# Kernel tuning notes

Hardware: AMD Instinct MI355X
Metric: run time of the kernel (lower is better)

## Reference

```python
import jax, jax.numpy as jnp
import numpy as np

DT = 1.0
TAU_MEM_INV = 0.05
V_LEAK = 0.0
V_TH = 1.0
ALPHA = 100.0  # norse SuperSpike surrogate slope


@jax.custom_vjp
def spike_fn(x):
    # heaviside forward, SuperSpike surrogate backward (norse default 'super')
    return (x > 0).astype(x.dtype)

def _spike_fwd(x):
    return spike_fn(x), x

def _spike_bwd(x, g):
    return (g / (ALPHA * jnp.abs(x) + 1.0) ** 2,)

spike_fn.defvjp(_spike_fwd, _spike_bwd)


def setup_inputs() -> dict:
    key = jax.random.key(0)
    ks = jax.random.split(key, 7)
    T, B = 100, 256
    sizes = [784, 64, 64, 10]
    inp = jax.random.normal(ks[0], (T, B, 1, sizes[0]), dtype=jnp.float32)
    out = {"inp": inp}
    for i in range(3):
        fan_in = sizes[i]
        out[f"W{i}"] = jax.random.normal(ks[1 + 2 * i], (sizes[i + 1], fan_in), dtype=jnp.float32) * (1.0 / np.sqrt(fan_in)).astype(np.float32)
        out[f"b{i}"] = jax.random.normal(ks[2 + 2 * i], (sizes[i + 1],), dtype=jnp.float32) * 0.01
    return out


def _snn_forward(inp, Ws, bs):
    x_seq = inp.squeeze(2)  # [T, B, 784]
    B = x_seq.shape[1]
    v0 = tuple(jnp.zeros((B, W.shape[0]), x_seq.dtype) for W in Ws)

    def step(vs, x):
        new_vs = []
        layer_sp = []
        for W, b, v in zip(Ws, bs, vs):
            i_cur = x @ W.T + b                                  # [B, out]
            v = v + DT * TAU_MEM_INV * (V_LEAK - v + i_cur)      # leaky integrate
            z = spike_fn(v - V_TH)                               # fire
            v = v - z * V_TH                                     # reset_subtract
            x = z
            new_vs.append(v)
            layer_sp.append(z.reshape(-1))                       # x.flatten() per layer
        return tuple(new_vs), (x, jnp.concatenate(layer_sp))

    _, (out_spikes, layer_spikes) = jax.lax.scan(step, v0, x_seq)
    # out_spikes: [T, B, 10]; layer_spikes flattened time-major like torch.cat(list)
    return out_spikes, layer_spikes.reshape(-1)


def reference(inp, W0, b0, W1, b1, W2, b2):
    return _snn_forward(inp, (W0, W1, W2), (b0, b1, b2))
```

## Files before the change

kernel.cpp:

```cpp
#include <hip/hip_runtime.h>

#define T_STEPS 100
#define BATCH 256
#define NIN 784
#define N0 64
#define N1 64
#define N2 10
#define CHUNK (BATCH*N0 + BATCH*N1 + BATCH*N2)
#define KPAD 800
#define WPLANE (N0*KPAD)
#define I0ELEMS (25600*64)

typedef __attribute__((ext_vector_type(8))) short short8;
typedef __attribute__((ext_vector_type(4))) float f32x4;

__device__ inline short bf16_rne(float x) {
  unsigned u = __float_as_uint(x);
  unsigned h = (u + 0x7FFFu + ((u >> 16) & 1u)) >> 16;
  return (short)h;
}
__device__ inline float bf16_val(short h) {
  return __uint_as_float(((unsigned)(unsigned short)h) << 16);
}

__global__ __launch_bounds__(256) void prep_w0(
    const float* __restrict__ W0, short* __restrict__ W0s) {
  int idx = blockIdx.x * 256 + threadIdx.x;
  int col = idx / KPAD, k = idx - col * KPAD;
  float w = (k < NIN) ? W0[col * NIN + k] : 0.0f;
  short h0 = bf16_rne(w);
  float r1 = w - bf16_val(h0);
  short h1 = bf16_rne(r1);
  float r2 = r1 - bf16_val(h1);
  short h2 = bf16_rne(r2);
  W0s[idx]              = h0;
  W0s[WPLANE + idx]     = h1;
  W0s[2 * WPLANE + idx] = h2;
}

__global__ __launch_bounds__(256, 3) void gemm0_kernel(
    const float* __restrict__ X, const short* __restrict__ W0s,
    const float* __restrict__ b0, float* __restrict__ I0T) {
  __shared__ float red[4][32][68];

  const int tid = threadIdx.x;
  const int r0  = blockIdx.x * 32;
  const int wid = tid >> 6;
  const int l   = tid & 63;
  const int lr  = l & 15;
  const int lk  = l >> 4;

  const int kbeg = wid * 192;
  const int ccnt = (wid < 3) ? 6 : 7;

  f32x4 acc[2][4];
#pragma unroll
  for (int rt = 0; rt < 2; ++rt)
#pragma unroll
    for (int ct = 0; ct < 4; ++ct) acc[rt][ct] = f32x4{0.f, 0.f, 0.f, 0.f};

  const float*  xr0 = X + (size_t)(r0 + lr) * NIN;
  const float*  xr1 = xr0 + 16 * NIN;
  const short8* wp  = (const short8*)W0s;

  for (int c = 0; c < ccnt; ++c) {
    const int kb = kbeg + c * 32;
    const int k0 = kb + lk * 8;

    float4 xa0, xb0, xa1, xb1;
    if (k0 < NIN) {
      xa0 = *(const float4*)(xr0 + k0);
      xb0 = *(const float4*)(xr0 + k0 + 4);
      xa1 = *(const float4*)(xr1 + k0);
      xb1 = *(const float4*)(xr1 + k0 + 4);
    } else {
      xa0 = xb0 = xa1 = xb1 = float4{0.f, 0.f, 0.f, 0.f};
    }

    short8 a0[3], a1[3];
    {
      float xs0[8] = {xa0.x, xa0.y, xa0.z, xa0.w, xb0.x, xb0.y, xb0.z, xb0.w};
      float xs1[8] = {xa1.x, xa1.y, xa1.z, xa1.w, xb1.x, xb1.y, xb1.z, xb1.w};
#pragma unroll
      for (int e = 0; e < 8; ++e) {
        float x  = xs0[e];
        short h0 = bf16_rne(x);   float rr1 = x - bf16_val(h0);
        short h1 = bf16_rne(rr1); float rr2 = rr1 - bf16_val(h1);
        a0[0][e] = h0; a0[1][e] = h1; a0[2][e] = bf16_rne(rr2);
        x  = xs1[e];
        h0 = bf16_rne(x);   rr1 = x - bf16_val(h0);
        h1 = bf16_rne(rr1); rr2 = rr1 - bf16_val(h1);
        a1[0][e] = h0; a1[1][e] = h1; a1[2][e] = bf16_rne(rr2);
      }
    }

    const int kof = kb / 8 + lk;
#pragma unroll
    for (int ct = 0; ct < 4; ++ct) {
      const size_t col = (size_t)(ct * 16 + lr);
      short8 bf0 = wp[        col * 100 + kof];
      short8 bf1 = wp[ 6400 + col * 100 + kof];
      short8 bf2 = wp[12800 + col * 100 + kof];
      {
        f32x4 a = acc[0][ct];
        a = __builtin_amdgcn_mfma_f32_16x16x32_bf16(a0[2], bf0, a, 0, 0, 0);
        a = __builtin_amdgcn_mfma_f32_16x16x32_bf16(a0[0], bf2, a, 0, 0, 0);
        a = __builtin_amdgcn_mfma_f32_16x16x32_bf16(a0[1], bf1, a, 0, 0, 0);
        a = __builtin_amdgcn_mfma_f32_16x16x32_bf16(a0[1], bf0, a, 0, 0, 0);
        a = __builtin_amdgcn_mfma_f32_16x16x32_bf16(a0[0], bf1, a, 0, 0, 0);
        a = __builtin_amdgcn_mfma_f32_16x16x32_bf16(a0[0], bf0, a, 0, 0, 0);
        acc[0][ct] = a;
      }
      {
        f32x4 a = acc[1][ct];
        a = __builtin_amdgcn_mfma_f32_16x16x32_bf16(a1[2], bf0, a, 0, 0, 0);
        a = __builtin_amdgcn_mfma_f32_16x16x32_bf16(a1[0], bf2, a, 0, 0, 0);
        a = __builtin_amdgcn_mfma_f32_16x16x32_bf16(a1[1], bf1, a, 0, 0, 0);
        a = __builtin_amdgcn_mfma_f32_16x16x32_bf16(a1[1], bf0, a, 0, 0, 0);
        a = __builtin_amdgcn_mfma_f32_16x16x32_bf16(a1[0], bf1, a, 0, 0, 0);
        a = __builtin_amdgcn_mfma_f32_16x16x32_bf16(a1[0], bf0, a, 0, 0, 0);
        acc[1][ct] = a;
      }
    }
  }

#pragma unroll
  for (int rt = 0; rt < 2; ++rt)
#pragma unroll
    for (int ct = 0; ct < 4; ++ct)
#pragma unroll
      for (int r = 0; r < 4; ++r)
        red[wid][rt * 16 + lk * 4 + r][ct * 16 + lr] = acc[rt][ct][r];
  __syncthreads();

  const int t0  = r0 >> 8;
  const int bb0 = r0 & 255;
  for (int idx = tid; idx < 32 * 16; idx += 256) {
    int row = idx >> 4, q = idx & 15;
    float4 v  = *(const float4*)&red[0][row][q * 4];
    float4 u1 = *(const float4*)&red[1][row][q * 4];
    float4 u2 = *(const float4*)&red[2][row][q * 4];
    float4 u3 = *(const float4*)&red[3][row][q * 4];
    v.x += u1.x; v.y += u1.y; v.z += u1.z; v.w += u1.w;
    v.x += u2.x; v.y += u2.y; v.z += u2.z; v.w += u2.w;
    v.x += u3.x; v.y += u3.y; v.z += u3.z; v.w += u3.w;
    float4 bv = ((const float4*)b0)[q];
    v.x += bv.x; v.y += bv.y; v.z += bv.z; v.w += bv.w;
    ((float4*)I0T)[((size_t)(bb0 + row) * T_STEPS + t0) * 16 + q] = v;
  }
}

__global__ __launch_bounds__(256) void fused_kernel(
    const float* __restrict__ I0T,
    const float* __restrict__ W1, const float* __restrict__ b1,
    const float* __restrict__ W2, const float* __restrict__ b2,
    float* __restrict__ out) {
  __shared__ float bufA[112][68];
  __shared__ float sW1t[64][68];
  __shared__ float sW2[N2][68];
  __shared__ float sI2[T_STEPS][N2];

  const int b   = blockIdx.x;
  const int tid = threadIdx.x;
  const int j   = tid & 63;
  const int tq  = tid >> 6;
  float* outSpk = out;
  float* laySpk = out + T_STEPS * BATCH * N2;

  {
    const float4* src = (const float4*)I0T + (size_t)b * (T_STEPS * 16);
    for (int idx = tid; idx < T_STEPS * 16; idx += 256) {
      float4 v = src[idx];
      int t = idx >> 4, j4 = idx & 15;
      *(float4*)&bufA[t][j4 * 4] = v;
    }
  }
  __syncthreads();

  if (tq == 0) {
    float v = 0.0f;
#pragma unroll
    for (int g = 0; g < 4; ++g) {
      float ic[25];
#pragma unroll
      for (int i = 0; i < 25; ++i) ic[i] = bufA[g * 25 + i][j];
#pragma unroll
      for (int i = 0; i < 25; ++i) {
        v = v + 0.05f * ((0.0f - v) + ic[i]);
        float z = (v > 1.0f) ? 1.0f : 0.0f;
        v -= z;
        ic[i] = z;
      }
#pragma unroll
      for (int i = 0; i < 25; ++i) bufA[g * 25 + i][j] = ic[i];
    }
  } else {
    for (int idx = tid - 64; idx < 64 * 16; idx += 192) {
      int i = idx >> 4, jv = idx & 15;
      float4 wv = *(const float4*)(W1 + (size_t)i * 64 + jv * 4);
      sW1t[jv * 4 + 0][i] = wv.x;
      sW1t[jv * 4 + 1][i] = wv.y;
      sW1t[jv * 4 + 2][i] = wv.z;
      sW1t[jv * 4 + 3][i] = wv.w;
    }
    for (int idx = tid - 64; idx < N2 * 16; idx += 192) {
      int o = idx >> 4, jv = idx & 15;
      *(float4*)&sW2[o][jv * 4] = *(const float4*)(W2 + (size_t)o * 64 + jv * 4);
    }
  }
  __syncthreads();

  for (int idx = tid; idx < T_STEPS * 16; idx += 256) {
    int t = idx >> 4, jv = idx & 15;
    *(float4*)(laySpk + (size_t)t * CHUNK + b * 64 + jv * 4) =
        *(const float4*)&bufA[t][jv * 4];
  }

  const int iq = tid & 15;
  const int ts = tid >> 4;
  float g1[4][7];
  {
    float4 bias = *(const float4*)(b1 + iq * 4);
#pragma unroll
    for (int tt = 0; tt < 7; ++tt) {
      g1[0][tt] = bias.x; g1[1][tt] = bias.y; g1[2][tt] = bias.z; g1[3][tt] = bias.w;
    }
#pragma unroll
    for (int jq = 0; jq < 16; ++jq) {
      float4 z4[7];
#pragma unroll
      for (int tt = 0; tt < 7; ++tt)
        z4[tt] = *(const float4*)&bufA[ts * 7 + tt][jq * 4];
      float4 w4[4];
#pragma unroll
      for (int e = 0; e < 4; ++e)
        w4[e] = *(const float4*)&sW1t[jq * 4 + e][iq * 4];
#pragma unroll
      for (int e = 0; e < 4; ++e) {
#pragma unroll
        for (int tt = 0; tt < 7; ++tt) {
          float zv = ((const float*)&z4[tt])[e];
          g1[0][tt] = fmaf(zv, w4[e].x, g1[0][tt]);
          g1[1][tt] = fmaf(zv, w4[e].y, g1[1][tt]);
          g1[2][tt] = fmaf(zv, w4[e].z, g1[2][tt]);
          g1[3][tt] = fmaf(zv, w4[e].w, g1[3][tt]);
        }
      }
    }
  }
  __syncthreads();
#pragma unroll
  for (int tt = 0; tt < 7; ++tt) {
    float4 o = {g1[0][tt], g1[1][tt], g1[2][tt], g1[3][tt]};
    *(float4*)&bufA[ts * 7 + tt][iq * 4] = o;
  }
  __syncthreads();

  if (tq == 0) {
    float v = 0.0f;
#pragma unroll
    for (int g = 0; g < 4; ++g) {
      float ic[25];
#pragma unroll
      for (int i = 0; i < 25; ++i) ic[i] = bufA[g * 25 + i][j];
#pragma unroll
      for (int i = 0; i < 25; ++i) {
        v = v + 0.05f * ((0.0f - v) + ic[i]);
        float z = (v > 1.0f) ? 1.0f : 0.0f;
        v -= z;
        ic[i] = z;
      }
#pragma unroll
      for (int i = 0; i < 25; ++i) bufA[g * 25 + i][j] = ic[i];
    }
  }
  __syncthreads();

  for (int idx = tid; idx < T_STEPS * 16; idx += 256) {
    int t = idx >> 4, jv = idx & 15;
    *(float4*)(laySpk + (size_t)t * CHUNK + BATCH * N0 + b * 64 + jv * 4) =
        *(const float4*)&bufA[t][jv * 4];
  }

  for (int idx = tid; idx < T_STEPS * N2; idx += 256) {
    int t = idx / N2, o = idx % N2;
    float a = b2[o];
#pragma unroll
    for (int jq = 0; jq < 16; ++jq) {
      float4 z = *(const float4*)&bufA[t][jq * 4];
      float4 wv = *(const float4*)&sW2[o][jq * 4];
      a += z.x * wv.x;
      a += z.y * wv.y;
      a += z.z * wv.z;
      a += z.w * wv.w;
    }
    sI2[t][o] = a;
  }
  __syncthreads();

  if (tid < N2) {
    float v = 0.0f;
#pragma unroll
    for (int g = 0; g < 4; ++g) {
      float ic[25];
#pragma unroll
      for (int i = 0; i < 25; ++i) ic[i] = sI2[g * 25 + i][tid];
#pragma unroll
      for (int i = 0; i < 25; ++i) {
        v = v + 0.05f * ((0.0f - v) + ic[i]);
        float z = (v > 1.0f) ? 1.0f : 0.0f;
        v -= z;
        ic[i] = z;
      }
#pragma unroll
      for (int i = 0; i < 25; ++i) sI2[g * 25 + i][tid] = ic[i];
    }
  }
  __syncthreads();

  for (int idx = tid; idx < T_STEPS * N2; idx += 256) {
    int t = idx / N2, o = idx % N2;
    float z = sI2[t][o];
    outSpk[(size_t)t * (BATCH * N2) + b * N2 + o] = z;
    laySpk[(size_t)t * CHUNK + BATCH * (N0 + N1) + b * N2 + o] = z;
  }
}

extern "C" void kernel_launch(void* const* d_in, const int* in_sizes, int n_in,
                              void* d_out, int out_size, void* d_ws, size_t ws_size,
                              hipStream_t stream) {
  const float* inp = (const float*)d_in[0];
  const float* W0  = (const float*)d_in[1];
  const float* b0  = (const float*)d_in[2];
  const float* W1  = (const float*)d_in[3];
  const float* b1  = (const float*)d_in[4];
  const float* W2  = (const float*)d_in[5];
  const float* b2  = (const float*)d_in[6];

  float* I0T = (float*)d_ws;
  short* W0s = (short*)(I0T + I0ELEMS);

  prep_w0<<<dim3(200), dim3(256), 0, stream>>>(W0, W0s);
  gemm0_kernel<<<dim3(800), dim3(256), 0, stream>>>(inp, W0s, b0, I0T);
  fused_kernel<<<dim3(BATCH), dim3(256), 0, stream>>>(I0T, W1, b1, W2, b2,
                                                      (float*)d_out);
}
```

Baseline: 62.31 us.

## Pre-pack W0 into MFMA fragment order and stage split X tiles through LDS

W0 is pre-split into three bf16 planes laid out in the exact per-lane MFMA fragment order, so each B-fragment load is one contiguous coalesced short8 per lane. The X rows are loaded with coalesced float4 accesses, split into bf16 hi/mid/lo parts, and written to a per-wave LDS tile. The next chunk's global load is issued before the MFMAs as a register prefetch. This adds LDS traffic and drops the occupancy hint on the launch bounds.

```diff
diff --git a/kernel.cpp b/kernel.cpp
--- a/kernel.cpp
+++ b/kernel.cpp
@@ -8,10 +8,14 @@
 #define N2 10
 #define CHUNK (BATCH*N0 + BATCH*N1 + BATCH*N2)
 #define KPAD 800
-#define WPLANE (N0*KPAD)
+#define NCH 25
 #define I0ELEMS (25600*64)
+#define AROW 40
+#define ASPL (32*AROW)
+#define AWAVE (3*ASPL)
 
 typedef __attribute__((ext_vector_type(8))) short short8;
+typedef __attribute__((ext_vector_type(4))) short short4v;
 typedef __attribute__((ext_vector_type(4))) float f32x4;
 
 __device__ inline short bf16_rne(float x) {
@@ -23,26 +27,32 @@
   return __uint_as_float(((unsigned)(unsigned short)h) << 16);
 }
 
-__global__ __launch_bounds__(256) void prep_w0(
-    const float* __restrict__ W0, short* __restrict__ W0s) {
+__global__ __launch_bounds__(256) void prep_w0_pack(
+    const float* __restrict__ W0, short* __restrict__ W0p) {
   int idx = blockIdx.x * 256 + threadIdx.x;
-  int col = idx / KPAD, k = idx - col * KPAD;
+  int e  = idx & 7;
+  int r1 = idx >> 3;
+  int l  = r1 & 63;
+  int r2 = r1 >> 6;
+  int ct = r2 & 3;
+  int r3 = r2 >> 2;
+  int p  = r3 % 3;
+  int c  = r3 / 3;
+  int k   = c * 32 + (l >> 4) * 8 + e;
+  int col = ct * 16 + (l & 15);
   float w = (k < NIN) ? W0[col * NIN + k] : 0.0f;
   short h0 = bf16_rne(w);
-  float r1 = w - bf16_val(h0);
-  short h1 = bf16_rne(r1);
-  float r2 = r1 - bf16_val(h1);
-  short h2 = bf16_rne(r2);
-  W0s[idx]              = h0;
-  W0s[WPLANE + idx]     = h1;
-  W0s[2 * WPLANE + idx] = h2;
-}
-
-__global__ __launch_bounds__(256, 3) void gemm0_kernel(
-    const float* __restrict__ X, const short* __restrict__ W0s,
+  float rr1 = w - bf16_val(h0);
+  short h1 = bf16_rne(rr1);
+  float rr2 = rr1 - bf16_val(h1);
+  short h2 = bf16_rne(rr2);
+  W0p[idx] = (p == 0) ? h0 : (p == 1) ? h1 : h2;
+}
+
+__global__ __launch_bounds__(256) void gemm0_kernel(
+    const float* __restrict__ X, const short* __restrict__ W0p,
     const float* __restrict__ b0, float* __restrict__ I0T) {
-  __shared__ float red[4][32][68];
-
+  __shared__ __align__(16) char smem[4 * 32 * 68 * 4];
   const int tid = threadIdx.x;
   const int r0  = blockIdx.x * 32;
   const int wid = tid >> 6;
@@ -50,8 +60,12 @@
   const int lr  = l & 15;
   const int lk  = l >> 4;
 
+  short* Aw = (short*)smem + wid * AWAVE;
+  float (*red)[32][68] = (float(*)[32][68])smem;
+
   const int kbeg = wid * 192;
   const int ccnt = (wid < 3) ? 6 : 7;
+  const int gbase = kbeg >> 5;
 
   f32x4 acc[2][4];
 #pragma unroll
@@ -59,70 +73,96 @@
 #pragma unroll
     for (int ct = 0; ct < 4; ++ct) acc[rt][ct] = f32x4{0.f, 0.f, 0.f, 0.f};
 
-  const float*  xr0 = X + (size_t)(r0 + lr) * NIN;
-  const float*  xr1 = xr0 + 16 * NIN;
-  const short8* wp  = (const short8*)W0s;
-
-  for (int c = 0; c < ccnt; ++c) {
-    const int kb = kbeg + c * 32;
-    const int k0 = kb + lk * 8;
-
-    float4 xa0, xb0, xa1, xb1;
-    if (k0 < NIN) {
-      xa0 = *(const float4*)(xr0 + k0);
-      xb0 = *(const float4*)(xr0 + k0 + 4);
-      xa1 = *(const float4*)(xr1 + k0);
-      xb1 = *(const float4*)(xr1 + k0 + 4);
-    } else {
-      xa0 = xb0 = xa1 = xb1 = float4{0.f, 0.f, 0.f, 0.f};
-    }
-
-    short8 a0[3], a1[3];
-    {
-      float xs0[8] = {xa0.x, xa0.y, xa0.z, xa0.w, xb0.x, xb0.y, xb0.z, xb0.w};
-      float xs1[8] = {xa1.x, xa1.y, xa1.z, xa1.w, xb1.x, xb1.y, xb1.z, xb1.w};
-#pragma unroll
-      for (int e = 0; e < 8; ++e) {
-        float x  = xs0[e];
+  const short8* wp8 = (const short8*)W0p;
+  const float4  z4  = {0.f, 0.f, 0.f, 0.f};
+
+  const int srow0 = l >> 3;
+  const int sks   = l & 7;
+
+  auto A_LOAD = [&](int kb, float4 xa[4]) {
+#pragma unroll
+    for (int i = 0; i < 4; ++i) {
+      int row = srow0 + i * 8;
+      int k   = kb + sks * 4;
+      xa[i] = (k < NIN) ? *(const float4*)(X + (size_t)(r0 + row) * NIN + k) : z4;
+    }
+  };
+  auto A_WRITE = [&](float4 xa[4]) {
+#pragma unroll
+    for (int i = 0; i < 4; ++i) {
+      int row = srow0 + i * 8;
+      float xs[4] = {xa[i].x, xa[i].y, xa[i].z, xa[i].w};
+      short4v v0, v1, v2;
+#pragma unroll
+      for (int e = 0; e < 4; ++e) {
+        float x  = xs[e];
         short h0 = bf16_rne(x);   float rr1 = x - bf16_val(h0);
         short h1 = bf16_rne(rr1); float rr2 = rr1 - bf16_val(h1);
-        a0[0][e] = h0; a0[1][e] = h1; a0[2][e] = bf16_rne(rr2);
-        x  = xs1[e];
-        h0 = bf16_rne(x);   rr1 = x - bf16_val(h0);
-        h1 = bf16_rne(rr1); rr2 = rr1 - bf16_val(h1);
-        a1[0][e] = h0; a1[1][e] = h1; a1[2][e] = bf16_rne(rr2);
-      }
-    }
-
-    const int kof = kb / 8 + lk;
+        v0[e] = h0; v1[e] = h1; v2[e] = bf16_rne(rr2);
+      }
+      short* base = Aw + row * AROW + sks * 4;
+      *(short4v*)(base)            = v0;
+      *(short4v*)(base + ASPL)     = v1;
+      *(short4v*)(base + 2 * ASPL) = v2;
+    }
+  };
+
+  {
+    float4 xa[4];
+    A_LOAD(kbeg, xa);
+    A_WRITE(xa);
+  }
+
+  for (int c = 0; c < ccnt; ++c) {
+    const bool more = (c + 1 < ccnt);
+    const int g = gbase + c;
+
+    short8 cb[4][3];
 #pragma unroll
     for (int ct = 0; ct < 4; ++ct) {
-      const size_t col = (size_t)(ct * 16 + lr);
-      short8 bf0 = wp[        col * 100 + kof];
-      short8 bf1 = wp[ 6400 + col * 100 + kof];
-      short8 bf2 = wp[12800 + col * 100 + kof];
+#pragma unroll
+      for (int p = 0; p < 3; ++p)
+        cb[ct][p] = wp8[(size_t)(((g * 3 + p) * 4 + ct)) * 64 + l];
+    }
+
+    float4 xn[4];
+    if (more) A_LOAD(kbeg + (c + 1) * 32, xn);
+
+    short8 af[2][3];
+#pragma unroll
+    for (int rti = 0; rti < 2; ++rti)
+#pragma unroll
+      for (int p = 0; p < 3; ++p)
+        af[rti][p] = *(const short8*)(Aw + p * ASPL + (rti * 16 + lr) * AROW + lk * 8);
+
+#pragma unroll
+    for (int ct = 0; ct < 4; ++ct) {
       {
         f32x4 a = acc[0][ct];
-        a = __builtin_amdgcn_mfma_f32_16x16x32_bf16(a0[2], bf0, a, 0, 0, 0);
-        a = __builtin_amdgcn_mfma_f32_16x16x32_bf16(a0[0], bf2, a, 0, 0, 0);
-        a = __builtin_amdgcn_mfma_f32_16x16x32_bf16(a0[1], bf1, a, 0, 0, 0);
-        a = __builtin_amdgcn_mfma_f32_16x16x32_bf16(a0[1], bf0, a, 0, 0, 0);
-        a = __builtin_amdgcn_mfma_f32_16x16x32_bf16(a0[0], bf1, a, 0, 0, 0);
-        a = __builtin_amdgcn_mfma_f32_16x16x32_bf16(a0[0], bf0, a, 0, 0, 0);
+        a = __builtin_amdgcn_mfma_f32_16x16x32_bf16(af[0][2], cb[ct][0], a, 0, 0, 0);
+        a = __builtin_amdgcn_mfma_f32_16x16x32_bf16(af[0][0], cb[ct][2], a, 0, 0, 0);
+        a = __builtin_amdgcn_mfma_f32_16x16x32_bf16(af[0][1], cb[ct][1], a, 0, 0, 0);
+        a = __builtin_amdgcn_mfma_f32_16x16x32_bf16(af[0][1], cb[ct][0], a, 0, 0, 0);
+        a = __builtin_amdgcn_mfma_f32_16x16x32_bf16(af[0][0], cb[ct][1], a, 0, 0, 0);
+        a = __builtin_amdgcn_mfma_f32_16x16x32_bf16(af[0][0], cb[ct][0], a, 0, 0, 0);
         acc[0][ct] = a;
       }
       {
         f32x4 a = acc[1][ct];
-        a = __builtin_amdgcn_mfma_f32_16x16x32_bf16(a1[2], bf0, a, 0, 0, 0);
-        a = __builtin_amdgcn_mfma_f32_16x16x32_bf16(a1[0], bf2, a, 0, 0, 0);
-        a = __builtin_amdgcn_mfma_f32_16x16x32_bf16(a1[1], bf1, a, 0, 0, 0);
-        a = __builtin_amdgcn_mfma_f32_16x16x32_bf16(a1[1], bf0, a, 0, 0, 0);
-        a = __builtin_amdgcn_mfma_f32_16x16x32_bf16(a1[0], bf1, a, 0, 0, 0);
-        a = __builtin_amdgcn_mfma_f32_16x16x32_bf16(a1[0], bf0, a, 0, 0, 0);
+        a = __builtin_amdgcn_mfma_f32_16x16x32_bf16(af[1][2], cb[ct][0], a, 0, 0, 0);
+        a = __builtin_amdgcn_mfma_f32_16x16x32_bf16(af[1][0], cb[ct][2], a, 0, 0, 0);
+        a = __builtin_amdgcn_mfma_f32_16x16x32_bf16(af[1][1], cb[ct][1], a, 0, 0, 0);
+        a = __builtin_amdgcn_mfma_f32_16x16x32_bf16(af[1][1], cb[ct][0], a, 0, 0, 0);
+        a = __builtin_amdgcn_mfma_f32_16x16x32_bf16(af[1][0], cb[ct][1], a, 0, 0, 0);
+        a = __builtin_amdgcn_mfma_f32_16x16x32_bf16(af[1][0], cb[ct][0], a, 0, 0, 0);
         acc[1][ct] = a;
       }
     }
-  }
+
+    if (more) A_WRITE(xn);
+  }
+
+  __syncthreads();
 
 #pragma unroll
   for (int rt = 0; rt < 2; ++rt)
@@ -338,10 +378,10 @@
   const float* b2  = (const float*)d_in[6];
 
   float* I0T = (float*)d_ws;
-  short* W0s = (short*)(I0T + I0ELEMS);
-
-  prep_w0<<<dim3(200), dim3(256), 0, stream>>>(W0, W0s);
-  gemm0_kernel<<<dim3(800), dim3(256), 0, stream>>>(inp, W0s, b0, I0T);
+  short* W0p = (short*)(I0T + I0ELEMS);
+
+  prep_w0_pack<<<dim3(600), dim3(256), 0, stream>>>(W0, W0p);
+  gemm0_kernel<<<dim3(800), dim3(256), 0, stream>>>(inp, W0p, b0, I0T);
   fused_kernel<<<dim3(BATCH), dim3(256), 0, stream>>>(I0T, W1, b1, W2, b2,
                                                       (float*)d_out);
 }
```

After: 65.25 us. 4.7% more time.
